# Kernel tuning notes

Measured on AMD Instinct MI355X. Metric: run time of the kernel, lower is better.

The kernel has to match this reference:

```python
import jax, jax.numpy as jnp
import numpy as np

N = 2048
IN_C, HID, LAT = 128, 128, 64
E_SPARSE = 65536


def gcn_conv(x, W, b, src, dst, w, n):
    # PyG GCNConv: h = D^-1/2 (A+I) D^-1/2 (x W) + b  (self-loops already in edge list)
    deg = jax.ops.segment_sum(w, dst, num_segments=n)
    dinv = jnp.where(deg > 0, jax.lax.rsqrt(deg), 0.0)
    norm = dinv[src] * w * dinv[dst]            # [E]
    h = x @ W                                   # [N, out]
    agg = jax.ops.segment_sum(h[src] * norm[:, None], dst, num_segments=n)
    return agg + b


def setup_inputs() -> dict:
    key = jax.random.key(0)
    ks = jax.random.split(key, 9)
    x = jax.random.normal(ks[0], (N, IN_C), jnp.float32)
    masked_y = jax.random.normal(ks[1], (N, N), jnp.float32)
    edge_index = jax.random.randint(ks[2], (2, E_SPARSE), 0, N, dtype=jnp.int32)
    s = 0.05
    W1 = jax.random.normal(ks[3], (IN_C, HID), jnp.float32) * s
    b1 = jnp.zeros((HID,), jnp.float32)
    Wmu = jax.random.normal(ks[4], (HID, LAT), jnp.float32) * s
    bmu = jnp.zeros((LAT,), jnp.float32)
    Wls = jax.random.normal(ks[5], (HID, LAT), jnp.float32) * s
    bls = jnp.zeros((LAT,), jnp.float32)
    return {"x": x, "masked_y": masked_y, "W1": W1, "b1": b1,
            "Wmu": Wmu, "bmu": bmu, "Wls": Wls, "bls": bls,
            "edge_index": edge_index}


def reference(x, masked_y, W1, b1, Wmu, bmu, Wls, bls, edge_index):
    n = x.shape[0]
    half = n // 2
    # masking leaves only the top-left [half, half] block of masked_y nonzero;
    # dense_to_sparse on that block -> all half*half (row, col) pairs (entries != 0 a.s.)
    rows = jnp.repeat(jnp.arange(half, dtype=edge_index.dtype), half)
    cols = jnp.tile(jnp.arange(half, dtype=edge_index.dtype), half)
    y_w = jax.nn.sigmoid(masked_y[:half, :half].reshape(-1))
    loop = jnp.arange(n, dtype=edge_index.dtype)
    src = jnp.concatenate([edge_index[0], rows, loop])
    dst = jnp.concatenate([edge_index[1], cols, loop])
    w = jnp.concatenate([jnp.ones((edge_index.shape[1],), x.dtype), y_w,
                         jnp.ones((n,), x.dtype)])
    hidden = jax.nn.relu(gcn_conv(x, W1, b1, src, dst, w, n))
    z_mu = gcn_conv(hidden, Wmu, bmu, src, dst, w, n)
    z_logstd = gcn_conv(hidden, Wls, bls, src, dst, w, n)
    return (z_mu, z_logstd)
```

## Files before the change

### kernel.cpp

```cpp
#include <hip/hip_runtime.h>

#define NN 2048
#define HALF 1024
#define CC 128
#define EE 65536
#define CAP 128

typedef unsigned short u16;

__device__ __forceinline__ float sigm(float v){ return 1.0f/(1.0f + __expf(-v)); }

__global__ __launch_bounds__(256) void k_prep(
    const float* __restrict__ my, const int* __restrict__ ei,
    float* __restrict__ SpRaw, float* __restrict__ colsum,
    int* __restrict__ cnt, u16* __restrict__ bucket)
{
  int b = blockIdx.x, t = threadIdx.x;
  if (b < 128) {
    int c0 = t*4;
    float cs0=0.f, cs1=0.f, cs2=0.f, cs3=0.f;
    #pragma unroll 2
    for (int rr=0; rr<8; ++rr){
      int r = b*8 + rr;
      float4 v = *(const float4*)(my + (size_t)r*NN + c0);
      float s0=sigm(v.x), s1=sigm(v.y), s2=sigm(v.z), s3=sigm(v.w);
      *(float4*)(SpRaw + (size_t)r*HALF + c0) = make_float4(s0,s1,s2,s3);
      cs0+=s0; cs1+=s1; cs2+=s2; cs3+=s3;
    }
    atomicAdd(&colsum[c0+0], cs0);
    atomicAdd(&colsum[c0+1], cs1);
    atomicAdd(&colsum[c0+2], cs2);
    atomicAdd(&colsum[c0+3], cs3);
  } else {
    int e = (b-128)*256 + t;
    int s = ei[e], d = ei[EE + e];
    int slot = atomicAdd(&cnt[d], 1);
    if (slot < CAP) bucket[d*CAP + slot] = (u16)s;
  }
}

__global__ __launch_bounds__(256) void k_dinv(const float* __restrict__ colsum,
                                              const int* __restrict__ cnt,
                                              float* __restrict__ dinv){
  int i = blockIdx.x*256 + threadIdx.x;
  float s = 1.0f + (float)cnt[i] + (i < HALF ? colsum[i] : 0.0f);
  dinv[i] = rsqrtf(s);
}

__global__ __launch_bounds__(256) void k_layer(
  const float* __restrict__ SpRaw, const float* __restrict__ F, const float* __restrict__ dinv,
  const int* __restrict__ cnt, const u16* __restrict__ bucket, float* __restrict__ AGG)
{
  int b = blockIdx.x, t = threadIdx.x;
  if (b < 256) {
    int f = t & 127, half = t >> 7;
    int dbase = (b>>2)*16 + half*8;
    int r0 = (b&3)*256;
    float acc[8];
    #pragma unroll
    for (int j=0;j<8;j++) acc[j] = 0.f;
    #pragma unroll 4
    for (int r=r0; r<r0+256; ++r){
      float fv = F[(size_t)r*CC + f] * dinv[r];
      const float4* sp4 = (const float4*)(SpRaw + (size_t)r*HALF + dbase);
      float4 s0 = sp4[0], s1 = sp4[1];
      acc[0] = fmaf(s0.x, fv, acc[0]);
      acc[1] = fmaf(s0.y, fv, acc[1]);
      acc[2] = fmaf(s0.z, fv, acc[2]);
      acc[3] = fmaf(s0.w, fv, acc[3]);
      acc[4] = fmaf(s1.x, fv, acc[4]);
      acc[5] = fmaf(s1.y, fv, acc[5]);
      acc[6] = fmaf(s1.z, fv, acc[6]);
      acc[7] = fmaf(s1.w, fv, acc[7]);
    }
    #pragma unroll
    for (int j=0;j<8;j++)
      atomicAdd(&AGG[(size_t)(dbase+j)*CC + f], acc[j]*dinv[dbase+j]);
  } else {
    int idx = b - 256;
    int d = idx*2 + (t>>7), f = t & 127;
    float dd = dinv[d];
    float acc = dd * F[(size_t)d*CC + f];
    int m = cnt[d]; m = m > CAP ? CAP : m;
    const u16* bk = bucket + d*CAP;
    for (int j=0;j<m;j++){
      int s = bk[j];
      acc = fmaf(dinv[s], F[(size_t)s*CC + f], acc);
    }
    atomicAdd(&AGG[(size_t)d*CC + f], dd*acc);
  }
}

__global__ __launch_bounds__(256) void k_hidden(
  const float* __restrict__ AGG, const float* __restrict__ W1, const float* __restrict__ b1,
  float* __restrict__ hid)
{
  __shared__ float la[8][CC];
  int t = threadIdx.x;
  int row0 = blockIdx.x*8;
  #pragma unroll
  for (int i=0;i<4;i++){
    int idx = i*256 + t;
    la[idx>>7][idx&127] = AGG[(size_t)row0*CC + idx];
  }
  __syncthreads();
  int f = t & 127, rh = t >> 7;
  float acc[4];
  float bb = b1[f];
  #pragma unroll
  for (int i=0;i<4;i++) acc[i] = bb;
  #pragma unroll 4
  for (int kk=0;kk<CC;kk++){
    float w = W1[kk*CC + f];
    #pragma unroll
    for (int i=0;i<4;i++) acc[i] = fmaf(la[rh*4+i][kk], w, acc[i]);
  }
  #pragma unroll
  for (int i=0;i<4;i++){
    float v = acc[i];
    hid[(size_t)(row0 + rh*4 + i)*CC + f] = v > 0.f ? v : 0.f;
  }
}

__global__ __launch_bounds__(256) void k_z(
  const float* __restrict__ AGG, const float* __restrict__ Wmu, const float* __restrict__ bmu,
  const float* __restrict__ Wls, const float* __restrict__ bls,
  float* __restrict__ out)
{
  __shared__ float la[8][CC];
  int t = threadIdx.x;
  int row0 = blockIdx.x*8;
  #pragma unroll
  for (int i=0;i<4;i++){
    int idx = i*256 + t;
    la[idx>>7][idx&127] = AGG[(size_t)row0*CC + idx];
  }
  __syncthreads();
  int f = t & 127, rh = t >> 7;
  const float* W = (f < 64) ? Wmu : Wls;
  int g = f & 63;
  float bb = (f < 64) ? bmu[g] : bls[g];
  size_t obase = (f < 64) ? 0 : (size_t)NN*64;
  float acc[4];
  #pragma unroll
  for (int i=0;i<4;i++) acc[i] = bb;
  #pragma unroll 4
  for (int kk=0;kk<CC;kk++){
    float w = W[kk*64 + g];
    #pragma unroll
    for (int i=0;i<4;i++) acc[i] = fmaf(la[rh*4+i][kk], w, acc[i]);
  }
  #pragma unroll
  for (int i=0;i<4;i++)
    out[obase + (size_t)(row0 + rh*4 + i)*64 + g] = acc[i];
}

extern "C" void kernel_launch(void* const* d_in, const int* in_sizes, int n_in,
                              void* d_out, int out_size, void* d_ws, size_t ws_size,
                              hipStream_t stream)
{
  (void)in_sizes; (void)n_in; (void)out_size; (void)ws_size;
  const float* x   = (const float*)d_in[0];
  const float* my  = (const float*)d_in[1];
  const float* W1  = (const float*)d_in[2];
  const float* b1  = (const float*)d_in[3];
  const float* Wmu = (const float*)d_in[4];
  const float* bmu = (const float*)d_in[5];
  const float* Wls = (const float*)d_in[6];
  const float* bls = (const float*)d_in[7];
  const int*   ei  = (const int*)d_in[8];
  float* out = (float*)d_out;
  char* ws = (char*)d_ws;

  float* colsum = (float*)(ws + 0);
  int*   cnt    = (int*)  (ws + 4096);
  float* AGG1   = (float*)(ws + 12288);
  float* AGG2   = (float*)(ws + 1060864);
  float* dinv   = (float*)(ws + 2109440);
  u16*   bucket = (u16*)  (ws + 2117632);
  float* SpRaw  = (float*)(ws + 2641920);
  float* hid    = (float*)(ws + 6836224);

  hipMemsetAsync(ws, 0, 2109440, stream);
  k_prep  <<<384,  256, 0, stream>>>(my, ei, SpRaw, colsum, cnt, bucket);
  k_dinv  <<<8,    256, 0, stream>>>(colsum, cnt, dinv);
  k_layer <<<1280, 256, 0, stream>>>(SpRaw, x,   dinv, cnt, bucket, AGG1);
  k_hidden<<<256,  256, 0, stream>>>(AGG1, W1, b1, hid);
  k_layer <<<1280, 256, 0, stream>>>(SpRaw, hid, dinv, cnt, bucket, AGG2);
  k_z     <<<256,  256, 0, stream>>>(AGG2, Wmu, bmu, Wls, bls, out);
}
```

Before: 178.9 us.

## Fuse aggregation with linear transforms and fold dinv into prep kernel

Merges the dense-block aggregation, sparse-edge aggregation and the following matmul (W1 or Wmu/Wls) into one kernel per layer. Each block now owns whole destination rows, so the atomic accumulation into AGG buffers and the separate hidden/z kernels go away. The dinv computation moves into the last block of k_prep via a done-counter, which removes one launch and shrinks the memset. In exchange each dense block loops over all 1024 source rows with 4 outputs per thread instead of splitting rows across 4 blocks, so there is less parallelism (128 dense blocks) and each thread runs a longer serial loop.

```diff
diff --git a/kernel.cpp b/kernel.cpp
--- a/kernel.cpp
+++ b/kernel.cpp
@@ -13,7 +13,8 @@
 __global__ __launch_bounds__(256) void k_prep(
     const float* __restrict__ my, const int* __restrict__ ei,
     float* __restrict__ SpRaw, float* __restrict__ colsum,
-    int* __restrict__ cnt, u16* __restrict__ bucket)
+    int* __restrict__ cnt, u16* __restrict__ bucket,
+    int* __restrict__ done, float* __restrict__ dinv)
 {
   int b = blockIdx.x, t = threadIdx.x;
   if (b < 128) {
@@ -37,122 +38,168 @@
     int slot = atomicAdd(&cnt[d], 1);
     if (slot < CAP) bucket[d*CAP + slot] = (u16)s;
   }
-}
-
-__global__ __launch_bounds__(256) void k_dinv(const float* __restrict__ colsum,
-                                              const int* __restrict__ cnt,
-                                              float* __restrict__ dinv){
-  int i = blockIdx.x*256 + threadIdx.x;
-  float s = 1.0f + (float)cnt[i] + (i < HALF ? colsum[i] : 0.0f);
-  dinv[i] = rsqrtf(s);
-}
-
-__global__ __launch_bounds__(256) void k_layer(
-  const float* __restrict__ SpRaw, const float* __restrict__ F, const float* __restrict__ dinv,
-  const int* __restrict__ cnt, const u16* __restrict__ bucket, float* __restrict__ AGG)
-{
+
+  __shared__ int lastf;
+  __syncthreads();
+  if (t == 0) {
+    int v = __hip_atomic_fetch_add(done, 1, __ATOMIC_ACQ_REL, __HIP_MEMORY_SCOPE_AGENT);
+    lastf = (v == 383) ? 1 : 0;
+  }
+  __syncthreads();
+  if (lastf) {
+    for (int i = t; i < NN; i += 256) {
+      int c = __hip_atomic_load(&cnt[i], __ATOMIC_RELAXED, __HIP_MEMORY_SCOPE_AGENT);
+      float cs = 0.f;
+      if (i < HALF)
+        cs = __hip_atomic_load(&colsum[i], __ATOMIC_RELAXED, __HIP_MEMORY_SCOPE_AGENT);
+      dinv[i] = rsqrtf(1.0f + (float)c + cs);
+    }
+  }
+}
+
+__global__ __launch_bounds__(256) void k_layer1(
+  const float* __restrict__ SpRaw, const float* __restrict__ x, const float* __restrict__ dinv,
+  const int* __restrict__ cnt, const u16* __restrict__ bucket,
+  const float* __restrict__ W1, const float* __restrict__ b1, float* __restrict__ hid)
+{
+  __shared__ float la[8][CC];
   int b = blockIdx.x, t = threadIdx.x;
-  if (b < 256) {
-    int f = t & 127, half = t >> 7;
-    int dbase = (b>>2)*16 + half*8;
-    int r0 = (b&3)*256;
-    float acc[8];
-    #pragma unroll
-    for (int j=0;j<8;j++) acc[j] = 0.f;
-    #pragma unroll 4
-    for (int r=r0; r<r0+256; ++r){
-      float fv = F[(size_t)r*CC + f] * dinv[r];
-      const float4* sp4 = (const float4*)(SpRaw + (size_t)r*HALF + dbase);
-      float4 s0 = sp4[0], s1 = sp4[1];
-      acc[0] = fmaf(s0.x, fv, acc[0]);
-      acc[1] = fmaf(s0.y, fv, acc[1]);
-      acc[2] = fmaf(s0.z, fv, acc[2]);
-      acc[3] = fmaf(s0.w, fv, acc[3]);
-      acc[4] = fmaf(s1.x, fv, acc[4]);
-      acc[5] = fmaf(s1.y, fv, acc[5]);
-      acc[6] = fmaf(s1.z, fv, acc[6]);
-      acc[7] = fmaf(s1.w, fv, acc[7]);
-    }
-    #pragma unroll
-    for (int j=0;j<8;j++)
-      atomicAdd(&AGG[(size_t)(dbase+j)*CC + f], acc[j]*dinv[dbase+j]);
+  int f = t & 127;
+  if (b < 128) {
+    int h = t >> 7;
+    int db = b*8 + h*4;
+    float acc[4] = {0.f,0.f,0.f,0.f};
+    #pragma unroll 4
+    for (int r=0; r<HALF; ++r){
+      float fv = x[(size_t)r*CC + f] * dinv[r];
+      float4 sp = *(const float4*)(SpRaw + (size_t)r*HALF + db);
+      acc[0] = fmaf(sp.x, fv, acc[0]);
+      acc[1] = fmaf(sp.y, fv, acc[1]);
+      acc[2] = fmaf(sp.z, fv, acc[2]);
+      acc[3] = fmaf(sp.w, fv, acc[3]);
+    }
+    #pragma unroll
+    for (int i=0;i<4;i++){
+      int d = db + i;
+      float dd = dinv[d];
+      float a = fmaf(dd, x[(size_t)d*CC + f], acc[i]);
+      int m = cnt[d]; m = m > CAP ? CAP : m;
+      const u16* bk = bucket + d*CAP;
+      for (int j=0;j<m;j++){
+        int s = bk[j];
+        a = fmaf(dinv[s], x[(size_t)s*CC + f], a);
+      }
+      la[h*4+i][f] = a * dd;
+    }
+    __syncthreads();
+    float o[4];
+    float bb = b1[f];
+    o[0]=bb; o[1]=bb; o[2]=bb; o[3]=bb;
+    #pragma unroll 4
+    for (int k=0;k<CC;k++){
+      float w = W1[k*CC + f];
+      o[0] = fmaf(la[h*4+0][k], w, o[0]);
+      o[1] = fmaf(la[h*4+1][k], w, o[1]);
+      o[2] = fmaf(la[h*4+2][k], w, o[2]);
+      o[3] = fmaf(la[h*4+3][k], w, o[3]);
+    }
+    #pragma unroll
+    for (int i=0;i<4;i++)
+      hid[(size_t)(db+i)*CC + f] = o[i] > 0.f ? o[i] : 0.f;
   } else {
-    int idx = b - 256;
-    int d = idx*2 + (t>>7), f = t & 127;
+    int rloc = t >> 7;
+    int d = HALF + (b-128)*2 + rloc;
     float dd = dinv[d];
-    float acc = dd * F[(size_t)d*CC + f];
+    float a = dd * x[(size_t)d*CC + f];
     int m = cnt[d]; m = m > CAP ? CAP : m;
     const u16* bk = bucket + d*CAP;
     for (int j=0;j<m;j++){
       int s = bk[j];
-      acc = fmaf(dinv[s], F[(size_t)s*CC + f], acc);
-    }
-    atomicAdd(&AGG[(size_t)d*CC + f], dd*acc);
-  }
-}
-
-__global__ __launch_bounds__(256) void k_hidden(
-  const float* __restrict__ AGG, const float* __restrict__ W1, const float* __restrict__ b1,
-  float* __restrict__ hid)
-{
-  __shared__ float la[8][CC];
-  int t = threadIdx.x;
-  int row0 = blockIdx.x*8;
-  #pragma unroll
-  for (int i=0;i<4;i++){
-    int idx = i*256 + t;
-    la[idx>>7][idx&127] = AGG[(size_t)row0*CC + idx];
-  }
-  __syncthreads();
-  int f = t & 127, rh = t >> 7;
-  float acc[4];
-  float bb = b1[f];
-  #pragma unroll
-  for (int i=0;i<4;i++) acc[i] = bb;
-  #pragma unroll 4
-  for (int kk=0;kk<CC;kk++){
-    float w = W1[kk*CC + f];
-    #pragma unroll
-    for (int i=0;i<4;i++) acc[i] = fmaf(la[rh*4+i][kk], w, acc[i]);
-  }
-  #pragma unroll
-  for (int i=0;i<4;i++){
-    float v = acc[i];
-    hid[(size_t)(row0 + rh*4 + i)*CC + f] = v > 0.f ? v : 0.f;
-  }
-}
-
-__global__ __launch_bounds__(256) void k_z(
-  const float* __restrict__ AGG, const float* __restrict__ Wmu, const float* __restrict__ bmu,
+      a = fmaf(dinv[s], x[(size_t)s*CC + f], a);
+    }
+    la[rloc][f] = a * dd;
+    __syncthreads();
+    float o = b1[f];
+    #pragma unroll 4
+    for (int k=0;k<CC;k++)
+      o = fmaf(la[rloc][k], W1[k*CC + f], o);
+    hid[(size_t)d*CC + f] = o > 0.f ? o : 0.f;
+  }
+}
+
+__global__ __launch_bounds__(256) void k_layer2(
+  const float* __restrict__ SpRaw, const float* __restrict__ hid, const float* __restrict__ dinv,
+  const int* __restrict__ cnt, const u16* __restrict__ bucket,
+  const float* __restrict__ Wmu, const float* __restrict__ bmu,
   const float* __restrict__ Wls, const float* __restrict__ bls,
   float* __restrict__ out)
 {
   __shared__ float la[8][CC];
-  int t = threadIdx.x;
-  int row0 = blockIdx.x*8;
-  #pragma unroll
-  for (int i=0;i<4;i++){
-    int idx = i*256 + t;
-    la[idx>>7][idx&127] = AGG[(size_t)row0*CC + idx];
-  }
-  __syncthreads();
-  int f = t & 127, rh = t >> 7;
+  int b = blockIdx.x, t = threadIdx.x;
+  int f = t & 127;
   const float* W = (f < 64) ? Wmu : Wls;
   int g = f & 63;
   float bb = (f < 64) ? bmu[g] : bls[g];
   size_t obase = (f < 64) ? 0 : (size_t)NN*64;
-  float acc[4];
-  #pragma unroll
-  for (int i=0;i<4;i++) acc[i] = bb;
-  #pragma unroll 4
-  for (int kk=0;kk<CC;kk++){
-    float w = W[kk*64 + g];
-    #pragma unroll
-    for (int i=0;i<4;i++) acc[i] = fmaf(la[rh*4+i][kk], w, acc[i]);
-  }
-  #pragma unroll
-  for (int i=0;i<4;i++)
-    out[obase + (size_t)(row0 + rh*4 + i)*64 + g] = acc[i];
+  if (b < 128) {
+    int h = t >> 7;
+    int db = b*8 + h*4;
+    float acc[4] = {0.f,0.f,0.f,0.f};
+    #pragma unroll 4
+    for (int r=0; r<HALF; ++r){
+      float fv = hid[(size_t)r*CC + f] * dinv[r];
+      float4 sp = *(const float4*)(SpRaw + (size_t)r*HALF + db);
+      acc[0] = fmaf(sp.x, fv, acc[0]);
+      acc[1] = fmaf(sp.y, fv, acc[1]);
+      acc[2] = fmaf(sp.z, fv, acc[2]);
+      acc[3] = fmaf(sp.w, fv, acc[3]);
+    }
+    #pragma unroll
+    for (int i=0;i<4;i++){
+      int d = db + i;
+      float dd = dinv[d];
+      float a = fmaf(dd, hid[(size_t)d*CC + f], acc[i]);
+      int m = cnt[d]; m = m > CAP ? CAP : m;
+      const u16* bk = bucket + d*CAP;
+      for (int j=0;j<m;j++){
+        int s = bk[j];
+        a = fmaf(dinv[s], hid[(size_t)s*CC + f], a);
+      }
+      la[h*4+i][f] = a * dd;
+    }
+    __syncthreads();
+    float o[4];
+    o[0]=bb; o[1]=bb; o[2]=bb; o[3]=bb;
+    #pragma unroll 4
+    for (int k=0;k<CC;k++){
+      float w = W[k*64 + g];
+      o[0] = fmaf(la[h*4+0][k], w, o[0]);
+      o[1] = fmaf(la[h*4+1][k], w, o[1]);
+      o[2] = fmaf(la[h*4+2][k], w, o[2]);
+      o[3] = fmaf(la[h*4+3][k], w, o[3]);
+    }
+    #pragma unroll
+    for (int i=0;i<4;i++)
+      out[obase + (size_t)(db+i)*64 + g] = o[i];
+  } else {
+    int rloc = t >> 7;
+    int d = HALF + (b-128)*2 + rloc;
+    float dd = dinv[d];
+    float a = dd * hid[(size_t)d*CC + f];
+    int m = cnt[d]; m = m > CAP ? CAP : m;
+    const u16* bk = bucket + d*CAP;
+    for (int j=0;j<m;j++){
+      int s = bk[j];
+      a = fmaf(dinv[s], hid[(size_t)s*CC + f], a);
+    }
+    la[rloc][f] = a * dd;
+    __syncthreads();
+    float o = bb;
+    #pragma unroll 4
+    for (int k=0;k<CC;k++)
+      o = fmaf(la[rloc][k], W[k*64 + g], o);
+    out[obase + (size_t)d*64 + g] = o;
+  }
 }
 
 extern "C" void kernel_launch(void* const* d_in, const int* in_sizes, int n_in,
@@ -172,20 +219,16 @@
   float* out = (float*)d_out;
   char* ws = (char*)d_ws;
 
-  float* colsum = (float*)(ws + 0);
-  int*   cnt    = (int*)  (ws + 4096);
-  float* AGG1   = (float*)(ws + 12288);
-  float* AGG2   = (float*)(ws + 1060864);
-  float* dinv   = (float*)(ws + 2109440);
-  u16*   bucket = (u16*)  (ws + 2117632);
-  float* SpRaw  = (float*)(ws + 2641920);
-  float* hid    = (float*)(ws + 6836224);
-
-  hipMemsetAsync(ws, 0, 2109440, stream);
-  k_prep  <<<384,  256, 0, stream>>>(my, ei, SpRaw, colsum, cnt, bucket);
-  k_dinv  <<<8,    256, 0, stream>>>(colsum, cnt, dinv);
-  k_layer <<<1280, 256, 0, stream>>>(SpRaw, x,   dinv, cnt, bucket, AGG1);
-  k_hidden<<<256,  256, 0, stream>>>(AGG1, W1, b1, hid);
-  k_layer <<<1280, 256, 0, stream>>>(SpRaw, hid, dinv, cnt, bucket, AGG2);
-  k_z     <<<256,  256, 0, stream>>>(AGG2, Wmu, bmu, Wls, bls, out);
-}
+  int*   cnt    = (int*)  (ws + 0);
+  float* colsum = (float*)(ws + 8192);
+  int*   done   = (int*)  (ws + 12288);
+  float* dinv   = (float*)(ws + 12352);
+  u16*   bucket = (u16*)  (ws + 20544);
+  float* SpRaw  = (float*)(ws + 544832);
+  float* hid    = (float*)(ws + 4739136);
+
+  hipMemsetAsync(ws, 0, 12352, stream);
+  k_prep  <<<384, 256, 0, stream>>>(my, ei, SpRaw, colsum, cnt, bucket, done, dinv);
+  k_layer1<<<640, 256, 0, stream>>>(SpRaw, x,   dinv, cnt, bucket, W1, b1, hid);
+  k_layer2<<<640, 256, 0, stream>>>(SpRaw, hid, dinv, cnt, bucket, Wmu, bmu, Wls, bls, out);
+}
```

New measurement: 348.7 us. 94.9% more time.

## Fuse dinv into prep via last-block flag and reorder GEMMs before aggregation

Applied to the files above, without the earlier changes.

The first layer's x·W1 moves into the prep kernel, and the second layer's Wmu/Wls projection is applied before aggregation (A·(hW) instead of (A·h)W). The separate dinv kernel is removed: the last block to finish prep, found through an atomic counter, computes dinv. The second aggregation accumulates straight into the output after it is pre-filled with biases, which drops one AGG buffer, the hidden and z kernels, and two launches. The cost is that the output is built by atomic accumulation, which changes floating-point summation order, and the last-block completion pattern depends on correct memory ordering.

```diff
diff --git a/kernel.cpp b/kernel.cpp
--- a/kernel.cpp
+++ b/kernel.cpp
@@ -11,10 +11,13 @@
 __device__ __forceinline__ float sigm(float v){ return 1.0f/(1.0f + __expf(-v)); }
 
 __global__ __launch_bounds__(256) void k_prep(
-    const float* __restrict__ my, const int* __restrict__ ei,
+    const float* __restrict__ my, const int* __restrict__ ei, const float* __restrict__ x,
+    const float* __restrict__ W1,
     float* __restrict__ SpRaw, float* __restrict__ colsum,
-    int* __restrict__ cnt, u16* __restrict__ bucket)
-{
+    int* __restrict__ cnt, u16* __restrict__ bucket,
+    int* __restrict__ done, float* __restrict__ dinv, float* __restrict__ H0)
+{
+  __shared__ float la[8][CC];
   int b = blockIdx.x, t = threadIdx.x;
   if (b < 128) {
     int c0 = t*4;
@@ -31,23 +34,53 @@
     atomicAdd(&colsum[c0+1], cs1);
     atomicAdd(&colsum[c0+2], cs2);
     atomicAdd(&colsum[c0+3], cs3);
-  } else {
+  } else if (b < 384) {
     int e = (b-128)*256 + t;
     int s = ei[e], d = ei[EE + e];
     int slot = atomicAdd(&cnt[d], 1);
     if (slot < CAP) bucket[d*CAP + slot] = (u16)s;
-  }
-}
-
-__global__ __launch_bounds__(256) void k_dinv(const float* __restrict__ colsum,
-                                              const int* __restrict__ cnt,
-                                              float* __restrict__ dinv){
-  int i = blockIdx.x*256 + threadIdx.x;
-  float s = 1.0f + (float)cnt[i] + (i < HALF ? colsum[i] : 0.0f);
-  dinv[i] = rsqrtf(s);
-}
-
-__global__ __launch_bounds__(256) void k_layer(
+  } else {
+    int row0 = (b-384)*8;
+    #pragma unroll
+    for (int i=0;i<4;i++){
+      int idx = i*256 + t;
+      la[idx>>7][idx&127] = x[(size_t)row0*CC + idx];
+    }
+    __syncthreads();
+    int f = t & 127, rh = t >> 7;
+    float o[4] = {0.f,0.f,0.f,0.f};
+    #pragma unroll 4
+    for (int k=0;k<CC;k++){
+      float w = W1[k*CC + f];
+      o[0] = fmaf(la[rh*4+0][k], w, o[0]);
+      o[1] = fmaf(la[rh*4+1][k], w, o[1]);
+      o[2] = fmaf(la[rh*4+2][k], w, o[2]);
+      o[3] = fmaf(la[rh*4+3][k], w, o[3]);
+    }
+    #pragma unroll
+    for (int i=0;i<4;i++)
+      H0[(size_t)(row0 + rh*4 + i)*CC + f] = o[i];
+  }
+
+  __shared__ int lastf;
+  __syncthreads();
+  if (t == 0) {
+    int v = __hip_atomic_fetch_add(done, 1, __ATOMIC_ACQ_REL, __HIP_MEMORY_SCOPE_AGENT);
+    lastf = (v == 639) ? 1 : 0;
+  }
+  __syncthreads();
+  if (lastf) {
+    for (int i = t; i < NN; i += 256) {
+      int c = __hip_atomic_load(&cnt[i], __ATOMIC_RELAXED, __HIP_MEMORY_SCOPE_AGENT);
+      float cs = 0.f;
+      if (i < HALF)
+        cs = __hip_atomic_load(&colsum[i], __ATOMIC_RELAXED, __HIP_MEMORY_SCOPE_AGENT);
+      dinv[i] = rsqrtf(1.0f + (float)c + cs);
+    }
+  }
+}
+
+__global__ __launch_bounds__(256) void k_layer1(
   const float* __restrict__ SpRaw, const float* __restrict__ F, const float* __restrict__ dinv,
   const int* __restrict__ cnt, const u16* __restrict__ bucket, float* __restrict__ AGG)
 {
@@ -91,68 +124,90 @@
   }
 }
 
-__global__ __launch_bounds__(256) void k_hidden(
-  const float* __restrict__ AGG, const float* __restrict__ W1, const float* __restrict__ b1,
-  float* __restrict__ hid)
+__global__ __launch_bounds__(256) void k_mid(
+  const float* __restrict__ AGG1, const float* __restrict__ b1,
+  const float* __restrict__ Wmu, const float* __restrict__ Wls,
+  const float* __restrict__ bmu, const float* __restrict__ bls,
+  float* __restrict__ G, float* __restrict__ out)
 {
   __shared__ float la[8][CC];
-  int t = threadIdx.x;
-  int row0 = blockIdx.x*8;
-  #pragma unroll
-  for (int i=0;i<4;i++){
-    int idx = i*256 + t;
-    la[idx>>7][idx&127] = AGG[(size_t)row0*CC + idx];
-  }
-  __syncthreads();
-  int f = t & 127, rh = t >> 7;
-  float acc[4];
-  float bb = b1[f];
-  #pragma unroll
-  for (int i=0;i<4;i++) acc[i] = bb;
-  #pragma unroll 4
-  for (int kk=0;kk<CC;kk++){
-    float w = W1[kk*CC + f];
-    #pragma unroll
-    for (int i=0;i<4;i++) acc[i] = fmaf(la[rh*4+i][kk], w, acc[i]);
-  }
-  #pragma unroll
-  for (int i=0;i<4;i++){
-    float v = acc[i];
-    hid[(size_t)(row0 + rh*4 + i)*CC + f] = v > 0.f ? v : 0.f;
-  }
-}
-
-__global__ __launch_bounds__(256) void k_z(
-  const float* __restrict__ AGG, const float* __restrict__ Wmu, const float* __restrict__ bmu,
-  const float* __restrict__ Wls, const float* __restrict__ bls,
-  float* __restrict__ out)
-{
-  __shared__ float la[8][CC];
-  int t = threadIdx.x;
-  int row0 = blockIdx.x*8;
-  #pragma unroll
-  for (int i=0;i<4;i++){
-    int idx = i*256 + t;
-    la[idx>>7][idx&127] = AGG[(size_t)row0*CC + idx];
-  }
-  __syncthreads();
-  int f = t & 127, rh = t >> 7;
-  const float* W = (f < 64) ? Wmu : Wls;
-  int g = f & 63;
-  float bb = (f < 64) ? bmu[g] : bls[g];
+  int b = blockIdx.x, t = threadIdx.x;
+  if (b < 256) {
+    int row0 = b*8;
+    #pragma unroll
+    for (int i=0;i<4;i++){
+      int idx = i*256 + t;
+      float v = AGG1[(size_t)row0*CC + idx] + b1[idx & 127];
+      la[idx>>7][idx&127] = v > 0.f ? v : 0.f;
+    }
+    __syncthreads();
+    int f = t & 127, rh = t >> 7;
+    int g = f & 63;
+    const float* W = (f < 64) ? Wmu : Wls;
+    float o[4] = {0.f,0.f,0.f,0.f};
+    #pragma unroll 4
+    for (int k=0;k<CC;k++){
+      float w = W[k*64 + g];
+      o[0] = fmaf(la[rh*4+0][k], w, o[0]);
+      o[1] = fmaf(la[rh*4+1][k], w, o[1]);
+      o[2] = fmaf(la[rh*4+2][k], w, o[2]);
+      o[3] = fmaf(la[rh*4+3][k], w, o[3]);
+    }
+    #pragma unroll
+    for (int i=0;i<4;i++)
+      G[(size_t)(row0 + rh*4 + i)*CC + f] = o[i];
+  } else {
+    int i = (b-256)*256 + t;
+    int g4 = (i & 15)*4;
+    const float* bb = (i < 32768) ? bmu : bls;
+    ((float4*)out)[i] = make_float4(bb[g4], bb[g4+1], bb[g4+2], bb[g4+3]);
+  }
+}
+
+__global__ __launch_bounds__(256) void k_layer2(
+  const float* __restrict__ SpRaw, const float* __restrict__ G, const float* __restrict__ dinv,
+  const int* __restrict__ cnt, const u16* __restrict__ bucket, float* __restrict__ out)
+{
+  int b = blockIdx.x, t = threadIdx.x;
+  int f = t & 127, g = f & 63;
   size_t obase = (f < 64) ? 0 : (size_t)NN*64;
-  float acc[4];
-  #pragma unroll
-  for (int i=0;i<4;i++) acc[i] = bb;
-  #pragma unroll 4
-  for (int kk=0;kk<CC;kk++){
-    float w = W[kk*64 + g];
-    #pragma unroll
-    for (int i=0;i<4;i++) acc[i] = fmaf(la[rh*4+i][kk], w, acc[i]);
-  }
-  #pragma unroll
-  for (int i=0;i<4;i++)
-    out[obase + (size_t)(row0 + rh*4 + i)*64 + g] = acc[i];
+  if (b < 256) {
+    int half = t >> 7;
+    int dbase = (b>>2)*16 + half*8;
+    int r0 = (b&3)*256;
+    float acc[8];
+    #pragma unroll
+    for (int j=0;j<8;j++) acc[j] = 0.f;
+    #pragma unroll 4
+    for (int r=r0; r<r0+256; ++r){
+      float fv = G[(size_t)r*CC + f] * dinv[r];
+      const float4* sp4 = (const float4*)(SpRaw + (size_t)r*HALF + dbase);
+      float4 s0 = sp4[0], s1 = sp4[1];
+      acc[0] = fmaf(s0.x, fv, acc[0]);
+      acc[1] = fmaf(s0.y, fv, acc[1]);
+      acc[2] = fmaf(s0.z, fv, acc[2]);
+      acc[3] = fmaf(s0.w, fv, acc[3]);
+      acc[4] = fmaf(s1.x, fv, acc[4]);
+      acc[5] = fmaf(s1.y, fv, acc[5]);
+      acc[6] = fmaf(s1.z, fv, acc[6]);
+      acc[7] = fmaf(s1.w, fv, acc[7]);
+    }
+    #pragma unroll
+    for (int j=0;j<8;j++)
+      atomicAdd(&out[obase + (size_t)(dbase+j)*64 + g], acc[j]*dinv[dbase+j]);
+  } else {
+    int idx = b - 256;
+    int d = idx*2 + (t>>7);
+    float dd = dinv[d];
+    float acc = dd * G[(size_t)d*CC + f];
+    int m = cnt[d]; m = m > CAP ? CAP : m;
+    const u16* bk = bucket + d*CAP;
+    for (int j=0;j<m;j++){
+      int s = bk[j];
+      acc = fmaf(dinv[s], G[(size_t)s*CC + f], acc);
+    }
+    atomicAdd(&out[obase + (size_t)d*64 + g], dd*acc);
+  }
 }
 
 extern "C" void kernel_launch(void* const* d_in, const int* in_sizes, int n_in,
@@ -172,20 +227,19 @@
   float* out = (float*)d_out;
   char* ws = (char*)d_ws;
 
-  float* colsum = (float*)(ws + 0);
-  int*   cnt    = (int*)  (ws + 4096);
-  float* AGG1   = (float*)(ws + 12288);
-  float* AGG2   = (float*)(ws + 1060864);
-  float* dinv   = (float*)(ws + 2109440);
-  u16*   bucket = (u16*)  (ws + 2117632);
-  float* SpRaw  = (float*)(ws + 2641920);
-  float* hid    = (float*)(ws + 6836224);
-
-  hipMemsetAsync(ws, 0, 2109440, stream);
-  k_prep  <<<384,  256, 0, stream>>>(my, ei, SpRaw, colsum, cnt, bucket);
-  k_dinv  <<<8,    256, 0, stream>>>(colsum, cnt, dinv);
-  k_layer <<<1280, 256, 0, stream>>>(SpRaw, x,   dinv, cnt, bucket, AGG1);
-  k_hidden<<<256,  256, 0, stream>>>(AGG1, W1, b1, hid);
-  k_layer <<<1280, 256, 0, stream>>>(SpRaw, hid, dinv, cnt, bucket, AGG2);
-  k_z     <<<256,  256, 0, stream>>>(AGG2, Wmu, bmu, Wls, bls, out);
-}
+  int*   cnt    = (int*)  (ws + 0);
+  float* colsum = (float*)(ws + 8192);
+  int*   done   = (int*)  (ws + 12288);
+  float* AGG1   = (float*)(ws + 12352);
+  float* dinv   = (float*)(ws + 1060928);
+  u16*   bucket = (u16*)  (ws + 1069120);
+  float* SpRaw  = (float*)(ws + 1593408);
+  float* H0     = (float*)(ws + 5787712);
+  float* G      = (float*)(ws + 6836288);
+
+  hipMemsetAsync(ws, 0, 1060928, stream);
+  k_prep  <<<640,  256, 0, stream>>>(my, ei, x, W1, SpRaw, colsum, cnt, bucket, done, dinv, H0);
+  k_layer1<<<1280, 256, 0, stream>>>(SpRaw, H0, dinv, cnt, bucket, AGG1);
+  k_mid   <<<512,  256, 0, stream>>>(AGG1, b1, Wmu, Wls, bmu, bls, G, out);
+  k_layer2<<<1280, 256, 0, stream>>>(SpRaw, G, dinv, cnt, bucket, out);
+}
```

Measured after the change: 188.3 us. 5.2% more time.
